# Performance work log

Hardware: AMD Instinct MI355X
Metric: run time of the kernel (lower is better)

The kernel has to match this reference:

```python
import jax, jax.numpy as jnp
import numpy as np

TAU = 0.1
EPS = 1e-8  # torch CosineSimilarity eps


def setup_inputs() -> dict:
    key = jax.random.key(0)
    k1, k2, k3 = jax.random.split(key, 3)
    B, D = 4096, 128
    z_i = jax.random.normal(k1, (B, D), dtype=jnp.float32)
    z_j = jax.random.normal(k2, (B, D), dtype=jnp.float32)
    y = jax.random.randint(k3, (B,), 0, 2)
    return {"z_i": z_i, "z_j": z_j, "y": y}


def reference(z_i, z_j, y):
    # p: (N, D) with N = 2B
    p = jnp.concatenate([z_i, z_j], axis=0)
    # cosine similarity via row-normalization + matmul (same math as the
    # broadcasted torch CosineSimilarity, without the O(N^2*D) intermediate)
    norm = jnp.maximum(jnp.linalg.norm(p, axis=1, keepdims=True), EPS)
    pn = p / norm
    sim = jnp.einsum('id,jd->ij', pn, pn) / TAU  # (N, N)

    N = sim.shape[0]
    y2 = jnp.concatenate([y, y], axis=0)
    eye = jnp.eye(N, dtype=sim.dtype)
    pos_mask = (y2[:, None] == y2[None, :]).astype(sim.dtype) * (1.0 - eye)
    logit_mask = 1.0 - eye

    # denominator excludes the diagonal (self-similarity)
    exp_logits = jnp.exp(sim) * logit_mask
    log_prob = sim - jnp.log(jnp.sum(exp_logits, axis=1, keepdims=True))
    mean_log_prob_pos = jnp.sum(pos_mask * log_prob, axis=1) / jnp.sum(pos_mask, axis=1)
    loss = -jnp.sum(mean_log_prob_pos)
    return loss
```

## Files before the change

### kernel.cpp

```cpp
#include <hip/hip_runtime.h>
#include <math.h>

#define BSZ 4096
#define NROW 8192
#define DIM 128
#define LOG2E10 14.426950408889634f

typedef __attribute__((ext_vector_type(8))) short bf16x8;
typedef __attribute__((ext_vector_type(4))) float f32x4;

#define PNH_F     (NROW * DIM / 2)
#define G_OFF     PNH_F
#define CNT_OFF   (G_OFF + 256)
#define SPART_OFF (G_OFF + 512)
#define PART_OFF  (SPART_OFF + 16 * NROW)

__device__ __forceinline__ unsigned short f2bf(float f) {
    unsigned u = __float_as_uint(f);
    return (unsigned short)((u + 0x7FFF + ((u >> 16) & 1)) >> 16);
}

__global__ void k_norm(const float* __restrict__ zi, const float* __restrict__ zj,
                       unsigned short* __restrict__ pnh, float* __restrict__ g) {
    int tid  = threadIdx.x;
    if (blockIdx.x == 0) g[tid] = 0.f;
    int wave = tid >> 6, lane = tid & 63;
    int row  = blockIdx.x * 4 + wave;
    const float* src = (row < BSZ) ? (zi + (size_t)row * DIM)
                                   : (zj + (size_t)(row - BSZ) * DIM);
    float2 v = ((const float2*)src)[lane];
    float ss = v.x * v.x + v.y * v.y;
    #pragma unroll
    for (int m = 32; m; m >>= 1) ss += __shfl_xor(ss, m, 64);
    float inv = 1.0f / fmaxf(sqrtf(ss), 1e-8f);
    unsigned short h0 = f2bf(v.x * inv), h1 = f2bf(v.y * inv);
    ((unsigned*)(pnh + (size_t)row * DIM))[lane] = (unsigned)h0 | ((unsigned)h1 << 16);
}

__global__ void k_colsum(const unsigned short* __restrict__ pnh, const int* __restrict__ y,
                         float* __restrict__ g, float* __restrict__ cnt) {
    __shared__ float red[4][4][64];
    int tid = threadIdx.x;
    if (blockIdx.x < 128) {
        int d2 = tid & 63;
        int rg = tid >> 6;
        int row0 = blockIdx.x * 64 + rg * 16;
        float s0a = 0.f, s0b = 0.f, s1a = 0.f, s1b = 0.f;
        #pragma unroll 4
        for (int i = 0; i < 16; ++i) {
            int r = row0 + i;
            unsigned u = ((const unsigned*)(pnh + (size_t)r * DIM))[d2];
            float va = __uint_as_float(u << 16);
            float vb = __uint_as_float(u & 0xFFFF0000u);
            if (y[r & (BSZ - 1)]) { s1a += va; s1b += vb; }
            else                  { s0a += va; s0b += vb; }
        }
        red[rg][0][d2] = s0a; red[rg][1][d2] = s0b;
        red[rg][2][d2] = s1a; red[rg][3][d2] = s1b;
        __syncthreads();
        int lab = tid >> 7, d = tid & 127;
        int which = lab * 2 + (d & 1), dd2 = d >> 1;
        float s = red[0][which][dd2] + red[1][which][dd2]
                + red[2][which][dd2] + red[3][which][dd2];
        atomicAdd(&g[lab * DIM + d], s);
    } else {
        __shared__ float r0[256];
        float c = 0.f;
        for (int r = tid; r < BSZ; r += 256) c += (float)y[r];
        r0[tid] = c;
        __syncthreads();
        for (int s = 128; s; s >>= 1) {
            if (tid < s) r0[tid] += r0[tid + s];
            __syncthreads();
        }
        if (tid == 0) { cnt[1] = 2.0f * r0[0]; cnt[0] = (float)NROW - 2.0f * r0[0]; }
    }
}

__global__ __launch_bounds__(256, 4)
void k_expsum(const unsigned short* __restrict__ pnh, float* __restrict__ spart) {
    __shared__ short bt[2][64 * 128];
    int tid  = threadIdx.x;
    int lane = tid & 63;
    int w    = tid >> 6;
    int l15 = lane & 15, q = lane >> 4;
    int rowBase = blockIdx.x * 128;
    int chunk   = blockIdx.y;
    int rwb     = rowBase + w * 32;

    bf16x8 a[2][4];
    const unsigned short* abase = pnh + (size_t)(rwb + l15) * DIM + q * 8;
    #pragma unroll
    for (int rf = 0; rf < 2; ++rf)
        #pragma unroll
        for (int ks = 0; ks < 4; ++ks)
            a[rf][ks] = *(const bf16x8*)(abase + (size_t)rf * 16 * DIM + ks * 32);

    float rs[2][4];
    #pragma unroll
    for (int rf = 0; rf < 2; ++rf)
        #pragma unroll
        for (int e = 0; e < 4; ++e) rs[rf][e] = 0.f;

    auto stage = [&](int s, int b) {
        const float4* src = (const float4*)(pnh + (size_t)(chunk * 512 + s * 64) * DIM);
        #pragma unroll
        for (int i = 0; i < 4; ++i) {
            int idx = tid + 256 * i;
            int row = idx >> 4, j = idx & 15;
            float4 v = src[idx];
            *(float4*)(&bt[b][row * 128 + ((j ^ (row & 15)) << 3)]) = v;
        }
    };

    stage(0, 0);
    __syncthreads();

    for (int s = 0; s < 8; ++s) {
        int cur = s & 1;
        if (s < 7) stage(s + 1, cur ^ 1);

        f32x4 acc[2][4];
        #pragma unroll
        for (int rf = 0; rf < 2; ++rf)
            #pragma unroll
            for (int c = 0; c < 4; ++c) acc[rf][c] = (f32x4){0.f, 0.f, 0.f, 0.f};

        const short* buf = bt[cur];
        #pragma unroll
        for (int ks = 0; ks < 4; ++ks)
            #pragma unroll
            for (int c = 0; c < 4; ++c) {
                bf16x8 bfrag = *(const bf16x8*)(buf + (c * 16 + l15) * 128 + (((ks * 4 + q) ^ l15) << 3));
                acc[0][c] = __builtin_amdgcn_mfma_f32_16x16x32_bf16(a[0][ks], bfrag, acc[0][c], 0, 0, 0);
                acc[1][c] = __builtin_amdgcn_mfma_f32_16x16x32_bf16(a[1][ks], bfrag, acc[1][c], 0, 0, 0);
            }

        int cb = chunk * 512 + s * 64;
        bool dia = (cb < rwb + 32) && (rwb < cb + 64);
        if (dia) {
            #pragma unroll
            for (int rf = 0; rf < 2; ++rf)
                #pragma unroll
                for (int c = 0; c < 4; ++c) {
                    int col = cb + c * 16 + l15;
                    #pragma unroll
                    for (int e = 0; e < 4; ++e) {
                        int row = rwb + rf * 16 + q * 4 + e;
                        float ex = exp2f(acc[rf][c][e] * LOG2E10);
                        if (row == col) ex = 0.f;
                        rs[rf][e] += ex;
                    }
                }
        } else {
            #pragma unroll
            for (int rf = 0; rf < 2; ++rf)
                #pragma unroll
                for (int c = 0; c < 4; ++c)
                    #pragma unroll
                    for (int e = 0; e < 4; ++e)
                        rs[rf][e] += exp2f(acc[rf][c][e] * LOG2E10);
        }
        __syncthreads();
    }

    #pragma unroll
    for (int rf = 0; rf < 2; ++rf)
        #pragma unroll
        for (int e = 0; e < 4; ++e) {
            float v = rs[rf][e];
            v += __shfl_xor(v, 1, 16);
            v += __shfl_xor(v, 2, 16);
            v += __shfl_xor(v, 4, 16);
            v += __shfl_xor(v, 8, 16);
            if (l15 == 0)
                spart[(size_t)chunk * NROW + rwb + rf * 16 + q * 4 + e] = v;
        }
}

__global__ void k_finalize(const unsigned short* __restrict__ pnh, const float* __restrict__ spart,
                           const float* __restrict__ g, const float* __restrict__ cnt,
                           const int* __restrict__ y, float* __restrict__ partial) {
    __shared__ float red[4];
    int tid = threadIdx.x, wv = tid >> 6, lane = tid & 63;
    int row = blockIdx.x * 4 + wv;
    int lab = y[row & (BSZ - 1)];
    unsigned u = ((const unsigned*)(pnh + (size_t)row * DIM))[lane];
    float p0 = __uint_as_float(u << 16);
    float p1 = __uint_as_float(u & 0xFFFF0000u);
    float2 gv = ((const float2*)(g + lab * DIM))[lane];
    float dg = p0 * gv.x + p1 * gv.y;
    float ds = p0 * p0 + p1 * p1;
    float sp = (lane < 16) ? spart[(size_t)lane * NROW + row] : 0.f;
    #pragma unroll
    for (int m = 32; m; m >>= 1) {
        dg += __shfl_xor(dg, m, 64);
        ds += __shfl_xor(ds, m, 64);
        sp += __shfl_xor(sp, m, 64);
    }
    if (lane == 0) {
        float C = cnt[lab] - 1.0f;
        float P = (dg - ds) * 10.0f;
        red[wv] = logf(sp) - P / C;
    }
    __syncthreads();
    if (tid == 0) partial[blockIdx.x] = red[0] + red[1] + red[2] + red[3];
}

__global__ void k_sum(const float* __restrict__ partial, float* __restrict__ out) {
    __shared__ float red[256];
    float v = 0.f;
    #pragma unroll
    for (int i = 0; i < 8; ++i) v += partial[threadIdx.x + 256 * i];
    red[threadIdx.x] = v;
    __syncthreads();
    for (int s = 128; s; s >>= 1) {
        if (threadIdx.x < s) red[threadIdx.x] += red[threadIdx.x + s];
        __syncthreads();
    }
    if (threadIdx.x == 0) out[0] = red[0];
}

extern "C" void kernel_launch(void* const* d_in, const int* in_sizes, int n_in,
                              void* d_out, int out_size, void* d_ws, size_t ws_size,
                              hipStream_t stream) {
    const float* zi = (const float*)d_in[0];
    const float* zj = (const float*)d_in[1];
    const int*   y  = (const int*)d_in[2];
    float* out = (float*)d_out;
    float* ws  = (float*)d_ws;

    unsigned short* pnh = (unsigned short*)ws;
    float* g       = ws + G_OFF;
    float* cnt     = ws + CNT_OFF;
    float* spart   = ws + SPART_OFF;
    float* partial = ws + PART_OFF;

    k_norm<<<NROW / 4, 256, 0, stream>>>(zi, zj, pnh, g);
    k_colsum<<<129, 256, 0, stream>>>(pnh, y, g, cnt);
    k_expsum<<<dim3(NROW / 128, 16), 256, 0, stream>>>(pnh, spart);
    k_finalize<<<NROW / 4, 256, 0, stream>>>(pnh, spart, g, cnt, y, partial);
    k_sum<<<1, 256, 0, stream>>>(partial, out);
}
```

Measured before the change: 105.1 us.

## Pre-swizzle normalized rows in global and retile expsum into 2x2 waves

The norm kernel now also writes a copy of the bf16 normalized rows in an XOR-swizzled order, so the expsum kernel can stage B tiles into LDS with plain contiguous float4 copies. Expsum is retiled: each wave covers 64 rows × 16 columns instead of 32 × 64, column chunks shrink to 256 with twice as many grid blocks, and the LDS buffer is halved. Per-row partial sums are stored row-major with 64 partials per row, so finalize reads them with a coalesced full-wave load. The cost is an extra global write of the swizzled copy, a larger workspace, and more A-fragment registers per wave.

New measurement: 157.0 us. 1.49x slower.

```diff
diff --git a/kernel.cpp b/kernel.cpp
--- a/kernel.cpp
+++ b/kernel.cpp
@@ -10,10 +10,10 @@
 typedef __attribute__((ext_vector_type(4))) float f32x4;
 
 #define PNH_F     (NROW * DIM / 2)
-#define G_OFF     PNH_F
+#define G_OFF     (2 * PNH_F)
 #define CNT_OFF   (G_OFF + 256)
 #define SPART_OFF (G_OFF + 512)
-#define PART_OFF  (SPART_OFF + 16 * NROW)
+#define PART_OFF  (SPART_OFF + 64 * NROW)
 
 __device__ __forceinline__ unsigned short f2bf(float f) {
     unsigned u = __float_as_uint(f);
@@ -21,7 +21,8 @@
 }
 
 __global__ void k_norm(const float* __restrict__ zi, const float* __restrict__ zj,
-                       unsigned short* __restrict__ pnh, float* __restrict__ g) {
+                       unsigned* __restrict__ pnh, unsigned* __restrict__ pnsw,
+                       float* __restrict__ g) {
     int tid  = threadIdx.x;
     if (blockIdx.x == 0) g[tid] = 0.f;
     int wave = tid >> 6, lane = tid & 63;
@@ -34,10 +35,14 @@
     for (int m = 32; m; m >>= 1) ss += __shfl_xor(ss, m, 64);
     float inv = 1.0f / fmaxf(sqrtf(ss), 1e-8f);
     unsigned short h0 = f2bf(v.x * inv), h1 = f2bf(v.y * inv);
-    ((unsigned*)(pnh + (size_t)row * DIM))[lane] = (unsigned)h0 | ((unsigned)h1 << 16);
-}
-
-__global__ void k_colsum(const unsigned short* __restrict__ pnh, const int* __restrict__ y,
+    unsigned pack = (unsigned)h0 | ((unsigned)h1 << 16);
+    pnh[(size_t)row * 64 + lane] = pack;
+    int j = lane >> 2;
+    int sw = ((j ^ (row & 15)) << 2) | (lane & 3);
+    pnsw[(size_t)row * 64 + sw] = pack;
+}
+
+__global__ void k_colsum(const unsigned* __restrict__ pnh, const int* __restrict__ y,
                          float* __restrict__ g, float* __restrict__ cnt) {
     __shared__ float red[4][4][64];
     int tid = threadIdx.x;
@@ -49,7 +54,7 @@
         #pragma unroll 4
         for (int i = 0; i < 16; ++i) {
             int r = row0 + i;
-            unsigned u = ((const unsigned*)(pnh + (size_t)r * DIM))[d2];
+            unsigned u = pnh[(size_t)r * 64 + d2];
             float va = __uint_as_float(u << 16);
             float vb = __uint_as_float(u & 0xFFFF0000u);
             if (y[r & (BSZ - 1)]) { s1a += va; s1b += vb; }
@@ -78,39 +83,38 @@
 }
 
 __global__ __launch_bounds__(256, 4)
-void k_expsum(const unsigned short* __restrict__ pnh, float* __restrict__ spart) {
-    __shared__ short bt[2][64 * 128];
+void k_expsum(const unsigned short* __restrict__ pnsw, float* __restrict__ spart) {
+    __shared__ short bt[2][32 * 128];
     int tid  = threadIdx.x;
     int lane = tid & 63;
     int w    = tid >> 6;
+    int wr = w & 1, wc = w >> 1;
     int l15 = lane & 15, q = lane >> 4;
     int rowBase = blockIdx.x * 128;
     int chunk   = blockIdx.y;
-    int rwb     = rowBase + w * 32;
-
-    bf16x8 a[2][4];
-    const unsigned short* abase = pnh + (size_t)(rwb + l15) * DIM + q * 8;
-    #pragma unroll
-    for (int rf = 0; rf < 2; ++rf)
+    int rwb     = rowBase + wr * 64;
+
+    bf16x8 a[4][4];
+    #pragma unroll
+    for (int rf = 0; rf < 4; ++rf) {
+        const unsigned short* ab = pnsw + (size_t)(rwb + rf * 16 + l15) * DIM;
         #pragma unroll
         for (int ks = 0; ks < 4; ++ks)
-            a[rf][ks] = *(const bf16x8*)(abase + (size_t)rf * 16 * DIM + ks * 32);
-
-    float rs[2][4];
-    #pragma unroll
-    for (int rf = 0; rf < 2; ++rf)
+            a[rf][ks] = *(const bf16x8*)(ab + (((ks * 4 + q) ^ l15) << 3));
+    }
+
+    float rs[4][4];
+    #pragma unroll
+    for (int rf = 0; rf < 4; ++rf)
         #pragma unroll
         for (int e = 0; e < 4; ++e) rs[rf][e] = 0.f;
 
     auto stage = [&](int s, int b) {
-        const float4* src = (const float4*)(pnh + (size_t)(chunk * 512 + s * 64) * DIM);
-        #pragma unroll
-        for (int i = 0; i < 4; ++i) {
-            int idx = tid + 256 * i;
-            int row = idx >> 4, j = idx & 15;
-            float4 v = src[idx];
-            *(float4*)(&bt[b][row * 128 + ((j ^ (row & 15)) << 3)]) = v;
-        }
+        const float4* src = (const float4*)(pnsw + (size_t)(chunk * 256 + s * 32) * DIM);
+        float4 v0 = src[tid];
+        float4 v1 = src[tid + 256];
+        ((float4*)bt[b])[tid]       = v0;
+        ((float4*)bt[b])[tid + 256] = v1;
     };
 
     stage(0, 0);
@@ -120,52 +124,45 @@
         int cur = s & 1;
         if (s < 7) stage(s + 1, cur ^ 1);
 
-        f32x4 acc[2][4];
-        #pragma unroll
-        for (int rf = 0; rf < 2; ++rf)
+        f32x4 acc[4];
+        #pragma unroll
+        for (int rf = 0; rf < 4; ++rf) acc[rf] = (f32x4){0.f, 0.f, 0.f, 0.f};
+
+        const short* buf = bt[cur];
+        #pragma unroll
+        for (int ks = 0; ks < 4; ++ks) {
+            bf16x8 bfrag = *(const bf16x8*)(buf + (wc * 16 + l15) * 128 + (((ks * 4 + q) ^ l15) << 3));
             #pragma unroll
-            for (int c = 0; c < 4; ++c) acc[rf][c] = (f32x4){0.f, 0.f, 0.f, 0.f};
-
-        const short* buf = bt[cur];
-        #pragma unroll
-        for (int ks = 0; ks < 4; ++ks)
-            #pragma unroll
-            for (int c = 0; c < 4; ++c) {
-                bf16x8 bfrag = *(const bf16x8*)(buf + (c * 16 + l15) * 128 + (((ks * 4 + q) ^ l15) << 3));
-                acc[0][c] = __builtin_amdgcn_mfma_f32_16x16x32_bf16(a[0][ks], bfrag, acc[0][c], 0, 0, 0);
-                acc[1][c] = __builtin_amdgcn_mfma_f32_16x16x32_bf16(a[1][ks], bfrag, acc[1][c], 0, 0, 0);
-            }
-
-        int cb = chunk * 512 + s * 64;
-        bool dia = (cb < rwb + 32) && (rwb < cb + 64);
+            for (int rf = 0; rf < 4; ++rf)
+                acc[rf] = __builtin_amdgcn_mfma_f32_16x16x32_bf16(a[rf][ks], bfrag, acc[rf], 0, 0, 0);
+        }
+
+        int cb = chunk * 256 + s * 32 + wc * 16;
+        bool dia = (cb < rwb + 64) && (rwb < cb + 16);
         if (dia) {
             #pragma unroll
-            for (int rf = 0; rf < 2; ++rf)
+            for (int rf = 0; rf < 4; ++rf) {
+                int col = cb + l15;
                 #pragma unroll
-                for (int c = 0; c < 4; ++c) {
-                    int col = cb + c * 16 + l15;
-                    #pragma unroll
-                    for (int e = 0; e < 4; ++e) {
-                        int row = rwb + rf * 16 + q * 4 + e;
-                        float ex = exp2f(acc[rf][c][e] * LOG2E10);
-                        if (row == col) ex = 0.f;
-                        rs[rf][e] += ex;
-                    }
+                for (int e = 0; e < 4; ++e) {
+                    int row = rwb + rf * 16 + q * 4 + e;
+                    float ex = exp2f(acc[rf][e] * LOG2E10);
+                    if (row == col) ex = 0.f;
+                    rs[rf][e] += ex;
                 }
+            }
         } else {
             #pragma unroll
-            for (int rf = 0; rf < 2; ++rf)
+            for (int rf = 0; rf < 4; ++rf)
                 #pragma unroll
-                for (int c = 0; c < 4; ++c)
-                    #pragma unroll
-                    for (int e = 0; e < 4; ++e)
-                        rs[rf][e] += exp2f(acc[rf][c][e] * LOG2E10);
-        }
-        __syncthreads();
-    }
-
-    #pragma unroll
-    for (int rf = 0; rf < 2; ++rf)
+                for (int e = 0; e < 4; ++e)
+                    rs[rf][e] += exp2f(acc[rf][e] * LOG2E10);
+        }
+        __syncthreads();
+    }
+
+    #pragma unroll
+    for (int rf = 0; rf < 4; ++rf)
         #pragma unroll
         for (int e = 0; e < 4; ++e) {
             float v = rs[rf][e];
@@ -174,24 +171,24 @@
             v += __shfl_xor(v, 4, 16);
             v += __shfl_xor(v, 8, 16);
             if (l15 == 0)
-                spart[(size_t)chunk * NROW + rwb + rf * 16 + q * 4 + e] = v;
-        }
-}
-
-__global__ void k_finalize(const unsigned short* __restrict__ pnh, const float* __restrict__ spart,
+                spart[(size_t)(rwb + rf * 16 + q * 4 + e) * 64 + chunk * 2 + wc] = v;
+        }
+}
+
+__global__ void k_finalize(const unsigned* __restrict__ pnh, const float* __restrict__ spart,
                            const float* __restrict__ g, const float* __restrict__ cnt,
                            const int* __restrict__ y, float* __restrict__ partial) {
     __shared__ float red[4];
     int tid = threadIdx.x, wv = tid >> 6, lane = tid & 63;
     int row = blockIdx.x * 4 + wv;
     int lab = y[row & (BSZ - 1)];
-    unsigned u = ((const unsigned*)(pnh + (size_t)row * DIM))[lane];
+    unsigned u = pnh[(size_t)row * 64 + lane];
     float p0 = __uint_as_float(u << 16);
     float p1 = __uint_as_float(u & 0xFFFF0000u);
     float2 gv = ((const float2*)(g + lab * DIM))[lane];
     float dg = p0 * gv.x + p1 * gv.y;
     float ds = p0 * p0 + p1 * p1;
-    float sp = (lane < 16) ? spart[(size_t)lane * NROW + row] : 0.f;
+    float sp = spart[(size_t)row * 64 + lane];
     #pragma unroll
     for (int m = 32; m; m >>= 1) {
         dg += __shfl_xor(dg, m, 64);
@@ -230,15 +227,16 @@
     float* out = (float*)d_out;
     float* ws  = (float*)d_ws;
 
-    unsigned short* pnh = (unsigned short*)ws;
+    unsigned* pnh   = (unsigned*)ws;
+    unsigned* pnsw  = (unsigned*)(ws + PNH_F);
     float* g       = ws + G_OFF;
     float* cnt     = ws + CNT_OFF;
     float* spart   = ws + SPART_OFF;
     float* partial = ws + PART_OFF;
 
-    k_norm<<<NROW / 4, 256, 0, stream>>>(zi, zj, pnh, g);
+    k_norm<<<NROW / 4, 256, 0, stream>>>(zi, zj, pnh, pnsw, g);
     k_colsum<<<129, 256, 0, stream>>>(pnh, y, g, cnt);
-    k_expsum<<<dim3(NROW / 128, 16), 256, 0, stream>>>(pnh, spart);
+    k_expsum<<<dim3(NROW / 128, 32), 256, 0, stream>>>((const unsigned short*)pnsw, spart);
     k_finalize<<<NROW / 4, 256, 0, stream>>>(pnh, spart, g, cnt, y, partial);
     k_sum<<<1, 256, 0, stream>>>(partial, out);
 }
```
